# Optimization experiments

Measured on AMD Instinct MI355X. Metric: run time of the kernel, lower is better.

## Reference

```python
import jax, jax.numpy as jnp
import numpy as np

D_MODEL = 1024  # scaling uses sqrt(d_model), as in the source


def setup_inputs() -> dict:
    key = jax.random.key(0)
    kx, kq, kk, kv = jax.random.split(key, 4)
    B, N, D, H = 4, 4096, D_MODEL, 128
    X = jax.random.normal(kx, (B, N, D), dtype=jnp.float32)
    # nn.Linear(d_model, d_head, bias=False) weights, stored as [d_model, d_head]
    s = 1.0 / np.sqrt(D)
    Wq = jax.random.normal(kq, (D, H), dtype=jnp.float32) * s
    Wk = jax.random.normal(kk, (D, H), dtype=jnp.float32) * s
    Wv = jax.random.normal(kv, (D, H), dtype=jnp.float32) * s
    return {"X": X, "Wq": Wq, "Wk": Wk, "Wv": Wv}


def reference(X, Wq, Wk, Wv):
    # Q, K, V: [B, N, H]
    Q = jnp.einsum("bnd,dh->bnh", X, Wq)
    K = jnp.einsum("bnd,dh->bnh", X, Wk)
    V = jnp.einsum("bnd,dh->bnh", X, Wv)
    # Scores: [B, N, N]; source divides by sqrt(d_model) (not sqrt(d_head))
    A = jnp.einsum("bqh,bkh->bqk", Q, K) / jnp.sqrt(jnp.float32(D_MODEL))
    A = jax.nn.softmax(A, axis=-1)
    # Dropout is identity in eval mode (deterministic reference baseline)
    return jnp.einsum("bqk,bkh->bqh", A, V)
```

## Files before the change

kernel.cpp:

```cpp
#include <hip/hip_runtime.h>
#include <stdint.h>

typedef __bf16 bf16_t;
typedef bf16_t bf16x8 __attribute__((ext_vector_type(8)));
typedef float f32x4 __attribute__((ext_vector_type(4)));
typedef float f32x16 __attribute__((ext_vector_type(16)));
typedef unsigned short u16;
typedef unsigned int u32;

#define MFMA16(a, b, c) __builtin_amdgcn_mfma_f32_16x16x32_bf16((a), (b), (c), 0, 0, 0)
#define MFMA32(a, b, c) __builtin_amdgcn_mfma_f32_32x32x16_bf16((a), (b), (c), 0, 0, 0)

#define QSCALE 0.04508422002778633f

__device__ __forceinline__ u16 f2bf(float f) {
  union { float f; unsigned u; } v; v.f = f;
  unsigned r = v.u + 0x7fffu + ((v.u >> 16) & 1u);
  return (u16)(r >> 16);
}

__device__ __forceinline__ float exp2x(float x) {
#if __has_builtin(__builtin_amdgcn_exp2f)
  return __builtin_amdgcn_exp2f(x);
#else
  return exp2f(x);
#endif
}

__device__ __forceinline__ float rcpx(float x) {
#if __has_builtin(__builtin_amdgcn_rcpf)
  return __builtin_amdgcn_rcpf(x);
#else
  return 1.0f / x;
#endif
}

__device__ __forceinline__ void async_cp16(const void* g, void* l) {
  __builtin_amdgcn_global_load_lds(
      (__attribute__((address_space(1))) void*)(void*)g,
      (__attribute__((address_space(3))) void*)l, 16, 0, 0);
}

__device__ __forceinline__ u32 cvtpk(float lo, float hi) {
  u32 r;
  asm("v_cvt_pk_bf16_f32 %0, %1, %2" : "=v"(r) : "v"(lo), "v"(hi));
  return r;
}
__device__ __forceinline__ void pl32swap(u32& a, u32& b) {
  asm volatile("v_permlane32_swap_b32 %0, %1" : "+v"(a), "+v"(b));
}

__global__ __launch_bounds__(256) void pack_w_k(const float* __restrict__ Wq,
                                                const float* __restrict__ Wk,
                                                const float* __restrict__ Wv,
                                                u16* __restrict__ wp) {
  int t = blockIdx.x * 256 + threadIdx.x;
  int mat = t >> 14;
  int rr = t & 16383;
  int frag = rr >> 6, lane = rr & 63;
  int nt = frag >> 5, kc = frag & 31;
  const float* W = (mat == 0) ? Wq : ((mat == 1) ? Wk : Wv);
  int k0 = kc * 32 + ((lane >> 4) << 3);
  int col = nt * 16 + (lane & 15);
  union { u16 h[8]; uint4 q; } u_;
#pragma unroll
  for (int j = 0; j < 8; ++j) u_.h[j] = f2bf(W[(size_t)(k0 + j) * 128 + col]);
  *(uint4*)(wp + (size_t)t * 8) = u_.q;
}

__device__ __forceinline__ void qkv_stage(const char* Xb, char* dst, int m0,
                                          int kc, int tid) {
#pragma unroll
  for (int i = 0; i < 2; ++i) {
    int p = i * 4096 + tid * 16;
    int row = p >> 8, cb = p & 255;
    int ucb = cb ^ ((row & 7) << 4);
    async_cp16(Xb + ((size_t)(m0 + row) * 4096 + (size_t)kc * 256 + ucb),
               dst + p);
  }
}

__global__ __launch_bounds__(256) void qkv_k(const float* __restrict__ X,
                                             const u16* __restrict__ wp,
                                             u16* __restrict__ Qb,
                                             u16* __restrict__ Kb,
                                             u16* __restrict__ Vt) {
  __shared__ __align__(16) char xs[2][8192];
  const int tid = threadIdx.x;
  const int w = tid >> 6, lane = tid & 63;
  const int r16 = lane >> 4, c16 = lane & 15;
  const int m0 = blockIdx.x * 32;
  const char* Xb = (const char*)X;

  f32x4 acc[2][6];
#pragma unroll
  for (int mt = 0; mt < 2; ++mt)
#pragma unroll
    for (int i = 0; i < 6; ++i) acc[mt][i] = (f32x4){0.f, 0.f, 0.f, 0.f};

  qkv_stage(Xb, xs[0], m0, 0, tid);
  qkv_stage(Xb, xs[1], m0, 1, tid);

  for (int kc = 0; kc < 16; ++kc) {
    if (kc + 1 < 16) {
      asm volatile("s_waitcnt vmcnt(2)" ::: "memory");
    } else {
      asm volatile("s_waitcnt vmcnt(0)" ::: "memory");
    }
    __builtin_amdgcn_s_barrier();
    asm volatile("" ::: "memory");

    const char* xb = xs[kc & 1];
    bf16x8 bw[6][2];
#pragma unroll
    for (int i = 0; i < 6; ++i) {
      int t = w + 4 * i;
      int mat = t >> 3, nt = t & 7;
      const u16* bp = wp + (size_t)mat * 131072 +
                      (size_t)((nt * 32 + kc * 2) * 64 + lane) * 8;
      bw[i][0] = *(const bf16x8*)(bp);
      bw[i][1] = *(const bf16x8*)(bp + 512);
    }
    bf16x8 a[2][2];
#pragma unroll
    for (int mt = 0; mt < 2; ++mt)
#pragma unroll
      for (int ks = 0; ks < 2; ++ks) {
        int row = mt * 16 + c16;
        int swz = (row & 7) << 4;
        int cb0 = ks * 128 + r16 * 32;
        f32x4 lo = *(const f32x4*)(xb + row * 256 + (cb0 ^ swz));
        f32x4 hi = *(const f32x4*)(xb + row * 256 + ((cb0 + 16) ^ swz));
        union { u32 u[4]; bf16x8 v; } pu;
        pu.u[0] = cvtpk(lo[0], lo[1]);
        pu.u[1] = cvtpk(lo[2], lo[3]);
        pu.u[2] = cvtpk(hi[0], hi[1]);
        pu.u[3] = cvtpk(hi[2], hi[3]);
        a[mt][ks] = pu.v;
      }
#pragma unroll
    for (int i = 0; i < 6; ++i)
#pragma unroll
      for (int ks = 0; ks < 2; ++ks)
#pragma unroll
        for (int mt = 0; mt < 2; ++mt)
          acc[mt][i] = MFMA16(a[mt][ks], bw[i][ks], acc[mt][i]);

    asm volatile("" ::: "memory");
    __builtin_amdgcn_s_barrier();
    asm volatile("" ::: "memory");
    if (kc + 2 < 16) qkv_stage(Xb, xs[kc & 1], m0, kc + 2, tid);
  }

  const int batch = m0 >> 12;
#pragma unroll
  for (int i = 0; i < 6; ++i) {
    int t = w + 4 * i;
    int mat = t >> 3, nt = t & 7;
#pragma unroll
    for (int mt = 0; mt < 2; ++mt) {
      f32x4 v = acc[mt][i];
      if (mat == 2) {
        int d = nt * 16 + c16;
        int nloc = (m0 & 4095) + mt * 16 + r16 * 4;
        union { u16 h[4]; uint2 q; } u_;
#pragma unroll
        for (int r = 0; r < 4; ++r) u_.h[r] = f2bf(v[r]);
        *(uint2*)(Vt + ((size_t)(batch * 128 + d)) * 4096 + nloc) = u_.q;
      } else {
        u16* dstm = (mat == 0) ? Qb : Kb;
        float sc = (mat == 0) ? QSCALE : 1.0f;
#pragma unroll
        for (int r = 0; r < 4; ++r) {
          int row = m0 + mt * 16 + r16 * 4 + r;
          dstm[(size_t)row * 128 + nt * 16 + c16] = f2bf(v[r] * sc);
        }
      }
    }
  }
}

#define STAGE_K(t)                                                        \
  {                                                                       \
    const char* s_ = kbase + (size_t)(t) * 16384;                         \
    char* d_ = smem + ((t) & 1) * 16384;                                  \
    _Pragma("unroll") for (int i_ = 0; i_ < 4; ++i_)                      \
        async_cp16(s_ + koff[i_], d_ + ldof[i_]);                         \
  }
#define STAGE_V(t)                                                        \
  {                                                                       \
    const char* s_ = vbase + (size_t)(t) * 128;                           \
    _Pragma("unroll") for (int i_ = 0; i_ < 4; ++i_)                      \
        async_cp16(s_ + voff[i_], vbuf + ldof[i_]);                       \
  }

__global__ __launch_bounds__(256, 3) void attn_k(const u16* __restrict__ Qb,
                                                 const u16* __restrict__ Kb,
                                                 const u16* __restrict__ Vt,
                                                 _Float16* __restrict__ Opart,
                                                 float* __restrict__ Ml,
                                                 int nsplit) {
  __shared__ __align__(16) char smem[49152];
  const int tid = threadIdx.x;
  const int w = tid >> 6, lane = tid & 63;
  const int l31 = lane & 31, hi = lane >> 5;

  const int B = gridDim.x;
  int xcd = blockIdx.x & 7, idx = blockIdx.x >> 3;
  int linear = xcd * (B >> 3) + idx;
  int qt = linear & 31, g = linear >> 5;
  int batch = g / nsplit, split = g - batch * nsplit;
  const int q0 = qt * 128;
  const int t0 = (split * 64) / nsplit;
  const int t1 = ((split + 1) * 64) / nsplit;
  const int T = t1 - t0;

  const char* kbase = (const char*)Kb + ((size_t)batch * 4096 + t0 * 64) * 256;
  const char* vbase = (const char*)Vt +
                      ((size_t)batch * 128 * 4096 + (size_t)t0 * 64) * 2;
  char* vbuf = smem + 32768;

  int koff[4], voff[4], ldof[4];
#pragma unroll
  for (int i = 0; i < 4; ++i) {
    int frag = i * 4 + w;
    int knt = frag >> 3, kkc = frag & 7;
    koff[i] = ((knt * 32 + l31) * 128 + kkc * 16 + hi * 8) * 2;
    int vks = frag >> 2, vdt = frag & 3;
    voff[i] = ((vdt * 32 + l31) * 4096 + vks * 16 + hi * 8) * 2;
    ldof[i] = i * 4096 + tid * 16;
  }

  bf16x8 qf[8];
  const u16* qrow = Qb + ((size_t)batch * 4096 + q0 + w * 32 + l31) * 128 + hi * 8;
#pragma unroll
  for (int kc = 0; kc < 8; ++kc) qf[kc] = *(const bf16x8*)(qrow + kc * 16);

  f32x16 acc[4];
#pragma unroll
  for (int dt = 0; dt < 4; ++dt)
#pragma unroll
    for (int j = 0; j < 16; ++j) acc[dt][j] = 0.f;
  float lacc[8];
#pragma unroll
  for (int i = 0; i < 8; ++i) lacc[i] = 0.f;

  STAGE_K(0);
  STAGE_V(0);
  if (T > 1) STAGE_K(1);

  for (int t = 0; t < T; ++t) {
    if (t + 1 < T) {
      asm volatile("s_waitcnt vmcnt(8)" ::: "memory");
    } else {
      asm volatile("s_waitcnt vmcnt(4)" ::: "memory");
    }
    __builtin_amdgcn_s_barrier();
    asm volatile("" ::: "memory");
    const char* kb = smem + (t & 1) * 16384;

    f32x16 sv[2];
    __builtin_amdgcn_s_setprio(1);
#pragma unroll
    for (int nt = 0; nt < 2; ++nt) {
      f32x16 s = {};
#pragma unroll
      for (int kc = 0; kc < 8; ++kc) {
        bf16x8 kf = *(const bf16x8*)(kb + (nt * 8 + kc) * 1024 + lane * 16);
        s = MFMA32(kf, qf[kc], s);
      }
      sv[nt] = s;
    }
    __builtin_amdgcn_s_setprio(0);

#pragma unroll
    for (int nt = 0; nt < 2; ++nt)
#pragma unroll
      for (int i = 0; i < 16; ++i) sv[nt][i] = exp2x(sv[nt][i]);
#pragma unroll
    for (int i = 0; i < 8; ++i)
      lacc[i] += (sv[0][i] + sv[0][i + 8]) + (sv[1][i] + sv[1][i + 8]);

    bf16x8 pf[4];
#pragma unroll
    for (int nt = 0; nt < 2; ++nt)
#pragma unroll
      for (int half = 0; half < 2; ++half) {
        const float* p = (const float*)&sv[nt] + half * 8;
        u32 a0 = cvtpk(p[0], p[1]);
        u32 b0 = cvtpk(p[4], p[5]);
        u32 c0 = cvtpk(p[2], p[3]);
        u32 d0 = cvtpk(p[6], p[7]);
        pl32swap(a0, b0);
        pl32swap(c0, d0);
        union { u32 u[4]; bf16x8 v; } pu;
        pu.u[0] = a0; pu.u[1] = c0; pu.u[2] = b0; pu.u[3] = d0;
        pf[nt * 2 + half] = pu.v;
      }

    if (t + 1 < T) {
      asm volatile("s_waitcnt vmcnt(4)" ::: "memory");
    } else {
      asm volatile("s_waitcnt vmcnt(0)" ::: "memory");
    }
    __builtin_amdgcn_s_barrier();
    asm volatile("" ::: "memory");

    __builtin_amdgcn_s_setprio(1);
#pragma unroll
    for (int dt = 0; dt < 4; ++dt) {
#pragma unroll
      for (int ks = 0; ks < 4; ++ks) {
        bf16x8 vf = *(const bf16x8*)(vbuf + (ks * 4 + dt) * 1024 + lane * 16);
        acc[dt] = MFMA32(pf[ks], vf, acc[dt]);
      }
    }
    __builtin_amdgcn_s_setprio(0);

    asm volatile("" ::: "memory");
    __builtin_amdgcn_s_barrier();
    asm volatile("" ::: "memory");

    if (t + 1 < T) STAGE_V(t + 1);
    if (t + 2 < T) STAGE_K(t + 2);
  }

  float ltot = ((lacc[0] + lacc[1]) + (lacc[2] + lacc[3])) +
               ((lacc[4] + lacc[5]) + (lacc[6] + lacc[7]));
  ltot += __shfl_xor(ltot, 32);

  size_t obase = (size_t)split * 16384 + (size_t)batch * 4096 + q0 + w * 32;
#pragma unroll
  for (int dt = 0; dt < 4; ++dt)
#pragma unroll
    for (int r = 0; r < 16; ++r) {
      int qr = (r & 3) + 8 * (r >> 2) + 4 * hi;
      float lq = __shfl(ltot, qr);
      Opart[(obase + qr) * 128 + dt * 32 + l31] = (_Float16)(acc[dt][r] * rcpx(lq));
    }
  if (lane < 32)
    Ml[(size_t)split * 16384 + (size_t)batch * 4096 + q0 + w * 32 + lane] = ltot;
}

template <int S>
__global__ __launch_bounds__(256) void reduce_k(const _Float16* __restrict__ Op,
                                                const float* __restrict__ Ml,
                                                float* __restrict__ Out) {
  int t = blockIdx.x * 256 + threadIdx.x;
  int q = t >> 4, d8 = (t & 15) << 3;
  float ls[S];
  float L = 0.f;
#pragma unroll
  for (int s = 0; s < S; ++s) {
    ls[s] = Ml[(size_t)s * 16384 + q];
    L += ls[s];
  }
  float o[8] = {0.f, 0.f, 0.f, 0.f, 0.f, 0.f, 0.f, 0.f};
#pragma unroll
  for (int s = 0; s < S; ++s) {
    union { uint4 u; _Float16 h[8]; } pv;
    pv.u = *(const uint4*)(Op + ((size_t)s * 16384 + q) * 128 + d8);
#pragma unroll
    for (int j = 0; j < 8; ++j) o[j] += (float)pv.h[j] * ls[s];
  }
  float inv = rcpx(L);
  float4 r0 = {o[0] * inv, o[1] * inv, o[2] * inv, o[3] * inv};
  float4 r1 = {o[4] * inv, o[5] * inv, o[6] * inv, o[7] * inv};
  *(float4*)(Out + (size_t)q * 128 + d8) = r0;
  *(float4*)(Out + (size_t)q * 128 + d8 + 4) = r1;
}

extern "C" void kernel_launch(void* const* d_in, const int* in_sizes, int n_in,
                              void* d_out, int out_size, void* d_ws, size_t ws_size,
                              hipStream_t stream) {
  const float* X  = (const float*)d_in[0];
  const float* Wq = (const float*)d_in[1];
  const float* Wk = (const float*)d_in[2];
  const float* Wv = (const float*)d_in[3];
  float* Out = (float*)d_out;
  char* ws = (char*)d_ws;
  u16* Qb = (u16*)(ws);
  u16* Kb = (u16*)(ws + (4u << 20));
  u16* Vt = (u16*)(ws + (8u << 20));
  u16* Wp = (u16*)(ws + (12u << 20));
  _Float16* Opart = (_Float16*)(ws + (13u << 20));

  int S = (ws_size >= (13ull << 20) + 6ull * (4194304ull + 65536ull)) ? 6 : 4;
  float* Ml = (float*)(ws + (13ull << 20) + (size_t)S * 4194304ull);

  pack_w_k<<<dim3(192), dim3(256), 0, stream>>>(Wq, Wk, Wv, Wp);
  qkv_k<<<dim3(512), dim3(256), 0, stream>>>(X, Wp, Qb, Kb, Vt);
  attn_k<<<dim3(128 * S), dim3(256), 0, stream>>>(Qb, Kb, Vt, Opart, Ml, S);
  if (S == 6)
    reduce_k<6><<<dim3(1024), dim3(256), 0, stream>>>(Opart, Ml, Out);
  else
    reduce_k<4><<<dim3(1024), dim3(256), 0, stream>>>(Opart, Ml, Out);
}
```

Before: 94.34 us.

## Pre-pack K and V into MFMA fragment order for contiguous async staging

Adds a pack kernel that reorders K and V from their row/transposed layouts into the exact per-lane fragment order the attention kernel loads into LDS. Each stage then copies 16 KB with fully contiguous coalesced 16-byte loads instead of strided gathers, and the per-thread offset registers go away. This costs an extra kernel launch plus a full read and write of K and V (about 8 MB), and the workspace is remapped so Opart overlaps the old Kb/Vt buffers once packing is done.

```diff
diff --git a/kernel.cpp b/kernel.cpp
--- a/kernel.cpp
+++ b/kernel.cpp
@@ -180,23 +180,35 @@
   }
 }
 
-#define STAGE_K(t)                                                        \
-  {                                                                       \
-    const char* s_ = kbase + (size_t)(t) * 16384;                         \
-    char* d_ = smem + ((t) & 1) * 16384;                                  \
-    _Pragma("unroll") for (int i_ = 0; i_ < 4; ++i_)                      \
-        async_cp16(s_ + koff[i_], d_ + ldof[i_]);                         \
-  }
-#define STAGE_V(t)                                                        \
-  {                                                                       \
-    const char* s_ = vbase + (size_t)(t) * 128;                           \
-    _Pragma("unroll") for (int i_ = 0; i_ < 4; ++i_)                      \
-        async_cp16(s_ + voff[i_], vbuf + ldof[i_]);                       \
-  }
+__global__ __launch_bounds__(256) void pack_kv_k(const u16* __restrict__ Kb,
+                                                 const u16* __restrict__ Vt,
+                                                 u16* __restrict__ Kf,
+                                                 u16* __restrict__ Vf) {
+  int t = blockIdx.x * 256 + threadIdx.x;
+  int lane = t & 63, l31 = lane & 31, hi = (lane >> 5) & 1;
+  if (t < 262144) {
+    int frag = t >> 6;
+    int batch = frag >> 10, kt = (frag >> 3) & 127, kc = frag & 7;
+    const u16* src = Kb + ((size_t)batch * 4096 + kt * 32 + l31) * 128 + kc * 16 + hi * 8;
+    *(uint4*)(Kf + (size_t)t * 8) = *(const uint4*)src;
+  } else {
+    int o = t - 262144;
+    int frag = o >> 6;
+    int batch = frag >> 10, tt = (frag >> 4) & 63, ks = (frag >> 2) & 3, dt = frag & 3;
+    const u16* src = Vt + ((size_t)batch * 128 + dt * 32 + l31) * 4096 + tt * 64 + ks * 16 + hi * 8;
+    *(uint4*)(Vf + (size_t)o * 8) = *(const uint4*)src;
+  }
+}
+
+__device__ __forceinline__ void stage16(const char* src, char* dst, int tid) {
+#pragma unroll
+  for (int i = 0; i < 4; ++i)
+    async_cp16(src + i * 4096 + tid * 16, dst + i * 4096 + tid * 16);
+}
 
 __global__ __launch_bounds__(256, 3) void attn_k(const u16* __restrict__ Qb,
-                                                 const u16* __restrict__ Kb,
-                                                 const u16* __restrict__ Vt,
+                                                 const u16* __restrict__ Kf,
+                                                 const u16* __restrict__ Vf,
                                                  _Float16* __restrict__ Opart,
                                                  float* __restrict__ Ml,
                                                  int nsplit) {
@@ -215,21 +227,9 @@
   const int t1 = ((split + 1) * 64) / nsplit;
   const int T = t1 - t0;
 
-  const char* kbase = (const char*)Kb + ((size_t)batch * 4096 + t0 * 64) * 256;
-  const char* vbase = (const char*)Vt +
-                      ((size_t)batch * 128 * 4096 + (size_t)t0 * 64) * 2;
+  const char* kfc = (const char*)Kf + (size_t)batch * 1048576 + (size_t)t0 * 16384;
+  const char* vfc = (const char*)Vf + (size_t)batch * 1048576 + (size_t)t0 * 16384;
   char* vbuf = smem + 32768;
-
-  int koff[4], voff[4], ldof[4];
-#pragma unroll
-  for (int i = 0; i < 4; ++i) {
-    int frag = i * 4 + w;
-    int knt = frag >> 3, kkc = frag & 7;
-    koff[i] = ((knt * 32 + l31) * 128 + kkc * 16 + hi * 8) * 2;
-    int vks = frag >> 2, vdt = frag & 3;
-    voff[i] = ((vdt * 32 + l31) * 4096 + vks * 16 + hi * 8) * 2;
-    ldof[i] = i * 4096 + tid * 16;
-  }
 
   bf16x8 qf[8];
   const u16* qrow = Qb + ((size_t)batch * 4096 + q0 + w * 32 + l31) * 128 + hi * 8;
@@ -245,9 +245,9 @@
 #pragma unroll
   for (int i = 0; i < 8; ++i) lacc[i] = 0.f;
 
-  STAGE_K(0);
-  STAGE_V(0);
-  if (T > 1) STAGE_K(1);
+  stage16(kfc, smem, tid);
+  stage16(vfc, vbuf, tid);
+  if (T > 1) stage16(kfc + 16384, smem + 16384, tid);
 
   for (int t = 0; t < T; ++t) {
     if (t + 1 < T) {
@@ -321,8 +321,8 @@
     __builtin_amdgcn_s_barrier();
     asm volatile("" ::: "memory");
 
-    if (t + 1 < T) STAGE_V(t + 1);
-    if (t + 2 < T) STAGE_K(t + 2);
+    if (t + 1 < T) stage16(vfc + (size_t)(t + 1) * 16384, vbuf, tid);
+    if (t + 2 < T) stage16(kfc + (size_t)(t + 2) * 16384, smem + (t & 1) * 16384, tid);
   }
 
   float ltot = ((lacc[0] + lacc[1]) + (lacc[2] + lacc[3])) +
@@ -380,17 +380,20 @@
   float* Out = (float*)d_out;
   char* ws = (char*)d_ws;
   u16* Qb = (u16*)(ws);
-  u16* Kb = (u16*)(ws + (4u << 20));
-  u16* Vt = (u16*)(ws + (8u << 20));
-  u16* Wp = (u16*)(ws + (12u << 20));
-  _Float16* Opart = (_Float16*)(ws + (13u << 20));
-
-  int S = (ws_size >= (13ull << 20) + 6ull * (4194304ull + 65536ull)) ? 6 : 4;
-  float* Ml = (float*)(ws + (13ull << 20) + (size_t)S * 4194304ull);
+  u16* Kf = (u16*)(ws + (4u << 20));
+  u16* Vf = (u16*)(ws + (8u << 20));
+  _Float16* Opart = (_Float16*)(ws + (12u << 20));
+  u16* Kb = (u16*)(ws + (12u << 20));
+  u16* Vt = (u16*)(ws + (16u << 20));
+  u16* Wp = (u16*)(ws + (20u << 20));
+
+  int S = (ws_size >= (12ull << 20) + 6ull * (4194304ull + 65536ull)) ? 6 : 4;
+  float* Ml = (float*)(ws + (12ull << 20) + (size_t)S * 4194304ull);
 
   pack_w_k<<<dim3(192), dim3(256), 0, stream>>>(Wq, Wk, Wv, Wp);
   qkv_k<<<dim3(512), dim3(256), 0, stream>>>(X, Wp, Qb, Kb, Vt);
-  attn_k<<<dim3(128 * S), dim3(256), 0, stream>>>(Qb, Kb, Vt, Opart, Ml, S);
+  pack_kv_k<<<dim3(2048), dim3(256), 0, stream>>>(Kb, Vt, Kf, Vf);
+  attn_k<<<dim3(128 * S), dim3(256), 0, stream>>>(Qb, Kf, Vf, Opart, Ml, S);
   if (S == 6)
     reduce_k<6><<<dim3(1024), dim3(256), 0, stream>>>(Opart, Ml, Out);
   else
```

After: 88.93 us. -5.7%, faster.
